# Kernel optimization log

Hardware: AMD Instinct MI355X
Metric: run time of the kernel (lower is better)

Reference implementation:

```python
import jax, jax.numpy as jnp
import numpy as np

NUM_OUT_POINTS = 2048  # matches init_kwargs num_out_points


def _fps_indices(x, m):
    """Farthest point sampling. x: [B, C, N] -> idx: [B, m] int32.
    Standard algorithm: seed at point 0, iteratively keep per-point min
    distance to the selected set and pick the argmax."""
    B, C, N = x.shape
    first = jnp.zeros((B,), dtype=jnp.int32)
    init_dists = jnp.full((B, N), jnp.inf, dtype=x.dtype)

    def body(carry, _):
        dists, last = carry                                   # [B,N], [B]
        last_pt = jnp.take_along_axis(x, last[:, None, None].astype(jnp.int32), axis=2)  # [B,C,1]
        d = jnp.sum((x - last_pt) ** 2, axis=1)               # [B,N] squared dist to newest point
        dists = jnp.minimum(dists, d)                         # min dist to selected set
        nxt = jnp.argmax(dists, axis=1).astype(jnp.int32)     # farthest point
        return (dists, nxt), nxt

    (_, _), rest = jax.lax.scan(body, (init_dists, first), None, length=m - 1)  # rest: [m-1, B]
    idx = jnp.concatenate([first[None, :], rest], axis=0)     # [m, B]
    return idx.T                                              # [B, m]


def setup_inputs() -> dict:
    key = jax.random.key(0)
    x = jax.random.normal(key, (32, 3, 131072), dtype=jnp.float32)
    return {"x": x}


def reference(x):
    # input_shape == output_shape == 'bcn', permute == False
    B, C, N = x.shape
    idx = _fps_indices(x, NUM_OUT_POINTS)                     # [B, M]
    gather_idx = jnp.broadcast_to(idx[:, None, :], (B, C, NUM_OUT_POINTS))
    y = jnp.take_along_axis(x, gather_idx, axis=2)            # [B, C, M]
    return y
```

## Files before the change

kernel.cpp:

```cpp
#include <hip/hip_runtime.h>
#include <stdint.h>


#define B_   32
#define N_   131072
#define M_   2048
#define WPB  8
#define T_   1024
#define PTS  16
#define ITERS (M_ - 1)
#define NPW  (N_ / WPB)

typedef unsigned long long u64;

__global__ void __launch_bounds__(T_, 4)
fps_main(const float* __restrict__ x, float* __restrict__ y,
         u64* __restrict__ slots) {
    const int bid  = blockIdx.x;
    const int b    = bid & (B_ - 1);
    const int wl   = bid >> 5;
    const int tid  = threadIdx.x;
    const int lane = tid & 63;
    const int wave = tid >> 6;

    const float* __restrict__ xb = x + (size_t)b * 3u * N_;
    float* __restrict__ yb = y + (size_t)b * 3u * M_;
    const unsigned pbase = (unsigned)(wl * NPW + tid);

    float X[PTS], Y[PTS], Z[PTS], D[PTS];
#pragma unroll
    for (int k = 0; k < PTS; ++k) {
        unsigned p = pbase + (unsigned)(k * T_);
        X[k] = xb[p];
        Y[k] = xb[N_ + p];
        Z[k] = xb[2 * N_ + p];
        D[k] = INFINITY;
    }

    float lx = xb[0], ly = xb[N_], lz = xb[2 * N_];
    if (wl == 0 && tid == 0) { yb[0] = lx; yb[M_] = ly; yb[2 * M_] = lz; }

    __shared__ u64   s_key[16];
    __shared__ float s_c[3];


    for (int it = 0; it < ITERS; ++it) {
        const int par = it & 1;

        float bv = -INFINITY; unsigned bi = 0u;
#pragma unroll
        for (int k = 0; k < PTS; ++k) {
            float dx = X[k] - lx;
            float dy = Y[k] - ly;
            float dz = Z[k] - lz;
            float d  = __fadd_rn(__fadd_rn(__fmul_rn(dx, dx), __fmul_rn(dy, dy)),
                                 __fmul_rn(dz, dz));
            float nd = fminf(D[k], d);
            D[k] = nd;
            bool t = nd > bv;
            bv = t ? nd : bv;
            bi = t ? (pbase + (unsigned)(k * T_)) : bi;
        }

        u64 key = ((u64)__float_as_uint(bv) << 32)
                | ((u64)(unsigned)it << 17)
                | (u64)(0x1FFFFu - bi);

#pragma unroll
        for (int off = 1; off < 64; off <<= 1) {
            u64 o = __shfl_xor(key, off);
            key = (o > key) ? o : key;
        }
        if (lane == 0) s_key[wave] = key;
        __syncthreads();

        if (wave == 0) {
            u64 k2 = (lane < 16) ? s_key[lane] : 0ull;
#pragma unroll
            for (int off = 1; off < 16; off <<= 1) {
                u64 o = __shfl_xor(k2, off);
                k2 = (o > k2) ? o : k2;
            }

            u64* base = slots + (size_t)((b * 2 + par) * WPB);
            if (lane == 0)
                __hip_atomic_store(base + wl, k2,
                                   __ATOMIC_RELAXED, __HIP_MEMORY_SCOPE_AGENT);

            const unsigned wtag = (unsigned)it;
            u64 got = 0ull;
            for (;;) {
                if (lane < WPB)
                    got = __hip_atomic_load(base + lane,
                                            __ATOMIC_RELAXED, __HIP_MEMORY_SCOPE_AGENT);
                bool ok = (lane >= WPB) | (((unsigned)(got >> 17) & 0x7FFFu) == wtag);
                if (__all(ok)) break;
                __builtin_amdgcn_s_sleep(2);
            }

            u64 w = (lane < WPB) ? got : 0ull;
#pragma unroll
            for (int off = 1; off < 8; off <<= 1) {
                u64 o = __shfl_xor(w, off);
                w = (o > w) ? o : w;
            }
            unsigned widx = 0x1FFFFu - (unsigned)(w & 0x1FFFFu);
            if (lane < 3) s_c[lane] = xb[(size_t)lane * N_ + widx];
        }
        __syncthreads();

        lx = s_c[0]; ly = s_c[1]; lz = s_c[2];
        if (wl == 0 && tid == 0) {
            yb[it + 1]          = lx;
            yb[M_ + it + 1]     = ly;
            yb[2 * M_ + it + 1] = lz;
        }
    }
}

extern "C" void kernel_launch(void* const* d_in, const int* in_sizes, int n_in,
                              void* d_out, int out_size, void* d_ws, size_t ws_size,
                              hipStream_t stream) {
    const float* x = (const float*)d_in[0];
    float* y = (float*)d_out;
    u64* slots = (u64*)d_ws;
    fps_main<<<B_ * WPB, T_, 0, stream>>>(x, y, slots);
}
```

Baseline: 5.579 ms.

## Replace block barriers with LDS flag sync and carry winner coordinates in records

The two __syncthreads per iteration are replaced by an LDS atomic counter that wave 0 spins on, plus a tag flag that the other waves spin on. Each block now publishes the winning point's coordinates together with its key in global slots, so the extra dependent global load of the winner's coordinates disappears. The s_sleep is also removed from the cross-block polling loop. Spin-waiting within a workgroup avoids barrier latency but burns issue slots and relies on the waves making forward progress. Polling 32 words instead of 8 adds memory traffic.

```diff
diff --git a/kernel.cpp b/kernel.cpp
--- a/kernel.cpp
+++ b/kernel.cpp
@@ -40,12 +40,17 @@
     float lx = xb[0], ly = xb[N_], lz = xb[2 * N_];
     if (wl == 0 && tid == 0) { yb[0] = lx; yb[M_] = ly; yb[2 * M_] = lz; }
 
-    __shared__ u64   s_key[16];
-    __shared__ float s_c[3];
+    __shared__ u64      s_rec[16][4];
+    __shared__ unsigned s_cnt;
+    __shared__ unsigned s_tag;
+    __shared__ float    s_c[3];
 
+    if (tid == 0) { s_cnt = 0u; s_tag = 0xFFFFFFFFu; }
+    __syncthreads();
 
     for (int it = 0; it < ITERS; ++it) {
         const int par = it & 1;
+        const unsigned ittag = (unsigned)it;
 
         float bv = -INFINITY; unsigned bi = 0u;
 #pragma unroll
@@ -63,57 +68,90 @@
         }
 
         u64 key = ((u64)__float_as_uint(bv) << 32)
-                | ((u64)(unsigned)it << 17)
+                | ((u64)ittag << 17)
                 | (u64)(0x1FFFFu - bi);
 
+        u64 wk = key;
 #pragma unroll
         for (int off = 1; off < 64; off <<= 1) {
-            u64 o = __shfl_xor(key, off);
-            key = (o > key) ? o : key;
+            u64 o = __shfl_xor(wk, off);
+            wk = (o > wk) ? o : wk;
         }
-        if (lane == 0) s_key[wave] = key;
-        __syncthreads();
+
+        if (key == wk) {
+            float bx = 0.f, by = 0.f, bz = 0.f;
+#pragma unroll
+            for (int k = 0; k < PTS; ++k)
+                if (pbase + (unsigned)(k * T_) == bi) { bx = X[k]; by = Y[k]; bz = Z[k]; }
+            s_rec[wave][0] = wk;
+            s_rec[wave][1] = ((u64)__float_as_uint(bx) << 32) | (u64)ittag;
+            s_rec[wave][2] = ((u64)__float_as_uint(by) << 32) | (u64)ittag;
+            s_rec[wave][3] = ((u64)__float_as_uint(bz) << 32) | (u64)ittag;
+            __hip_atomic_fetch_add(&s_cnt, 1u, __ATOMIC_RELEASE, __HIP_MEMORY_SCOPE_WORKGROUP);
+        }
 
         if (wave == 0) {
-            u64 k2 = (lane < 16) ? s_key[lane] : 0ull;
+            const unsigned want = 16u * (unsigned)(it + 1);
+            while (__hip_atomic_load(&s_cnt, __ATOMIC_ACQUIRE,
+                                     __HIP_MEMORY_SCOPE_WORKGROUP) < want) {}
+
+            u64 k2 = (lane < 16) ? s_rec[lane][0] : 0ull;
+            u64 m2 = k2;
 #pragma unroll
             for (int off = 1; off < 16; off <<= 1) {
-                u64 o = __shfl_xor(k2, off);
-                k2 = (o > k2) ? o : k2;
+                u64 o = __shfl_xor(m2, off);
+                m2 = (o > m2) ? o : m2;
+            }
+            u64 ball = __ballot(lane < 16 && k2 == m2);
+            int wv = __ffsll(ball) - 1;
+
+            u64* grec = slots + (size_t)(((b * 2 + par) * WPB + wl) * 4);
+            u64 word = 0ull;
+            if (lane == 0)      word = m2;
+            else if (lane < 4)  word = s_rec[wv][lane];
+            if (lane < 4)
+                __hip_atomic_store(&grec[lane], word,
+                                   __ATOMIC_RELAXED, __HIP_MEMORY_SCOPE_AGENT);
+
+            u64* gb = slots + (size_t)((b * 2 + par) * WPB * 4);
+            const int w = lane & 3;
+            u64 got = 0ull;
+            for (;;) {
+                if (lane < 32)
+                    got = __hip_atomic_load(&gb[lane],
+                                            __ATOMIC_RELAXED, __HIP_MEMORY_SCOPE_AGENT);
+                bool ok = (lane >= 32) |
+                          ((w == 0) ? (((unsigned)(got >> 17) & 0x7FFFu) == ittag)
+                                    : (((unsigned)got & 0x7FFFu) == ittag));
+                if (__all(ok)) break;
             }
 
-            u64* base = slots + (size_t)((b * 2 + par) * WPB);
-            if (lane == 0)
-                __hip_atomic_store(base + wl, k2,
-                                   __ATOMIC_RELAXED, __HIP_MEMORY_SCOPE_AGENT);
+            u64 kk = (lane < 32 && w == 0) ? got : 0ull;
+#pragma unroll
+            for (int off = 1; off < 64; off <<= 1) {
+                u64 o = __shfl_xor(kk, off);
+                kk = (o > kk) ? o : kk;
+            }
+            u64 ball2 = __ballot(lane < 32 && w == 0 && got == kk);
+            int winl = __ffsll(ball2) - 1;
+            lx = __uint_as_float((unsigned)(__shfl(got, winl + 1) >> 32));
+            ly = __uint_as_float((unsigned)(__shfl(got, winl + 2) >> 32));
+            lz = __uint_as_float((unsigned)(__shfl(got, winl + 3) >> 32));
 
-            const unsigned wtag = (unsigned)it;
-            u64 got = 0ull;
-            for (;;) {
-                if (lane < WPB)
-                    got = __hip_atomic_load(base + lane,
-                                            __ATOMIC_RELAXED, __HIP_MEMORY_SCOPE_AGENT);
-                bool ok = (lane >= WPB) | (((unsigned)(got >> 17) & 0x7FFFu) == wtag);
-                if (__all(ok)) break;
-                __builtin_amdgcn_s_sleep(2);
+            if (lane == 0) {
+                s_c[0] = lx; s_c[1] = ly; s_c[2] = lz;
+                __hip_atomic_store(&s_tag, ittag,
+                                   __ATOMIC_RELEASE, __HIP_MEMORY_SCOPE_WORKGROUP);
             }
-
-            u64 w = (lane < WPB) ? got : 0ull;
-#pragma unroll
-            for (int off = 1; off < 8; off <<= 1) {
-                u64 o = __shfl_xor(w, off);
-                w = (o > w) ? o : w;
+        } else {
+            while (__hip_atomic_load(&s_tag, __ATOMIC_ACQUIRE,
+                                     __HIP_MEMORY_SCOPE_WORKGROUP) != ittag) {}
+            lx = s_c[0]; ly = s_c[1]; lz = s_c[2];
+            if (wl == 0 && wave == 1 && lane == 0) {
+                yb[it + 1]          = lx;
+                yb[M_ + it + 1]     = ly;
+                yb[2 * M_ + it + 1] = lz;
             }
-            unsigned widx = 0x1FFFFu - (unsigned)(w & 0x1FFFFu);
-            if (lane < 3) s_c[lane] = xb[(size_t)lane * N_ + widx];
-        }
-        __syncthreads();
-
-        lx = s_c[0]; ly = s_c[1]; lz = s_c[2];
-        if (wl == 0 && tid == 0) {
-            yb[it + 1]          = lx;
-            yb[M_ + it + 1]     = ly;
-            yb[2 * M_ + it + 1] = lz;
         }
     }
 }
```

Measured after the change: 8.026 ms. +43.9%, slower.

## Interleave two batches per workgroup to hide cross-block sync latency

Applied to the files above, without the earlier changes.

Each workgroup now handles two batch elements (b and b+16), with 16 workgroups per batch pair instead of 8 per batch. The per-iteration global slot publish for batch A happens before computing batch B, so the cross-workgroup handshake latency of one batch can overlap the compute of the other. The grid size stays at 256 workgroups but the split per batch doubles, which widens the spin-wait fan-in to 16 slots. The spin sleep is also shortened.

```diff
diff --git a/kernel.cpp b/kernel.cpp
--- a/kernel.cpp
+++ b/kernel.cpp
@@ -2,118 +2,177 @@
 #include <stdint.h>
 
 
-#define B_   32
-#define N_   131072
-#define M_   2048
-#define WPB  8
-#define T_   1024
-#define PTS  16
+#define B_    32
+#define N_    131072
+#define M_    2048
+#define PAIRS 16
+#define WPB   16
+#define T_    1024
+#define PTS   8
 #define ITERS (M_ - 1)
-#define NPW  (N_ / WPB)
+#define NPW   (N_ / WPB)
 
 typedef unsigned long long u64;
+
+__device__ __forceinline__ u64 wave_max64(u64 v) {
+#pragma unroll
+    for (int off = 1; off < 64; off <<= 1) {
+        u64 o = __shfl_xor(v, off);
+        v = (o > v) ? o : v;
+    }
+    return v;
+}
 
 __global__ void __launch_bounds__(T_, 4)
 fps_main(const float* __restrict__ x, float* __restrict__ y,
          u64* __restrict__ slots) {
-    const int bid  = blockIdx.x;
-    const int b    = bid & (B_ - 1);
-    const int wl   = bid >> 5;
+    const int wg   = blockIdx.x;
+    const int pp   = wg & (PAIRS - 1);
+    const int wl   = wg >> 4;
+    const int bA   = pp;
+    const int bB   = pp + PAIRS;
     const int tid  = threadIdx.x;
     const int lane = tid & 63;
     const int wave = tid >> 6;
 
-    const float* __restrict__ xb = x + (size_t)b * 3u * N_;
-    float* __restrict__ yb = y + (size_t)b * 3u * M_;
+    const float* __restrict__ xA = x + (size_t)bA * 3u * N_;
+    const float* __restrict__ xB = x + (size_t)bB * 3u * N_;
+    float* __restrict__ yA = y + (size_t)bA * 3u * M_;
+    float* __restrict__ yB = y + (size_t)bB * 3u * M_;
     const unsigned pbase = (unsigned)(wl * NPW + tid);
 
-    float X[PTS], Y[PTS], Z[PTS], D[PTS];
+    float XA[PTS], YA[PTS], ZA[PTS], DA[PTS];
+    float XB[PTS], YB[PTS], ZB[PTS], DB[PTS];
 #pragma unroll
     for (int k = 0; k < PTS; ++k) {
         unsigned p = pbase + (unsigned)(k * T_);
-        X[k] = xb[p];
-        Y[k] = xb[N_ + p];
-        Z[k] = xb[2 * N_ + p];
-        D[k] = INFINITY;
+        XA[k] = xA[p]; YA[k] = xA[N_ + p]; ZA[k] = xA[2*N_ + p]; DA[k] = INFINITY;
+        XB[k] = xB[p]; YB[k] = xB[N_ + p]; ZB[k] = xB[2*N_ + p]; DB[k] = INFINITY;
     }
 
-    float lx = xb[0], ly = xb[N_], lz = xb[2 * N_];
-    if (wl == 0 && tid == 0) { yb[0] = lx; yb[M_] = ly; yb[2 * M_] = lz; }
+    float lxA = xA[0], lyA = xA[N_], lzA = xA[2*N_];
+    float lxB = xB[0], lyB = xB[N_], lzB = xB[2*N_];
+    if (wl == 0 && tid == 0) {
+        yA[0] = lxA; yA[M_] = lyA; yA[2*M_] = lzA;
+        yB[0] = lxB; yB[M_] = lyB; yB[2*M_] = lzB;
+    }
 
-    __shared__ u64   s_key[16];
-    __shared__ float s_c[3];
+    __shared__ u64   s_keyA[16], s_keyB[16];
+    __shared__ float s_cA[3], s_cB[3];
 
 
     for (int it = 0; it < ITERS; ++it) {
         const int par = it & 1;
+        const unsigned ittag = (unsigned)it;
 
-        float bv = -INFINITY; unsigned bi = 0u;
+        {
+            float bv = -INFINITY; unsigned bi = 0u;
 #pragma unroll
-        for (int k = 0; k < PTS; ++k) {
-            float dx = X[k] - lx;
-            float dy = Y[k] - ly;
-            float dz = Z[k] - lz;
-            float d  = __fadd_rn(__fadd_rn(__fmul_rn(dx, dx), __fmul_rn(dy, dy)),
-                                 __fmul_rn(dz, dz));
-            float nd = fminf(D[k], d);
-            D[k] = nd;
-            bool t = nd > bv;
-            bv = t ? nd : bv;
-            bi = t ? (pbase + (unsigned)(k * T_)) : bi;
+            for (int k = 0; k < PTS; ++k) {
+                float dx = XA[k]-lxA, dy = YA[k]-lyA, dz = ZA[k]-lzA;
+                float d  = __fadd_rn(__fadd_rn(__fmul_rn(dx,dx), __fmul_rn(dy,dy)),
+                                     __fmul_rn(dz,dz));
+                float nd = fminf(DA[k], d);
+                DA[k] = nd;
+                bool t = nd > bv;
+                bv = t ? nd : bv;
+                bi = t ? (pbase + (unsigned)(k * T_)) : bi;
+            }
+            u64 key = ((u64)__float_as_uint(bv) << 32)
+                    | ((u64)ittag << 17) | (u64)(0x1FFFFu - bi);
+            key = wave_max64(key);
+            if (lane == 0) s_keyA[wave] = key;
         }
-
-        u64 key = ((u64)__float_as_uint(bv) << 32)
-                | ((u64)(unsigned)it << 17)
-                | (u64)(0x1FFFFu - bi);
-
-#pragma unroll
-        for (int off = 1; off < 64; off <<= 1) {
-            u64 o = __shfl_xor(key, off);
-            key = (o > key) ? o : key;
-        }
-        if (lane == 0) s_key[wave] = key;
         __syncthreads();
 
         if (wave == 0) {
-            u64 k2 = (lane < 16) ? s_key[lane] : 0ull;
+            u64 k2 = (lane < 16) ? s_keyA[lane] : 0ull;
 #pragma unroll
             for (int off = 1; off < 16; off <<= 1) {
                 u64 o = __shfl_xor(k2, off);
                 k2 = (o > k2) ? o : k2;
             }
+            if (lane == 0)
+                __hip_atomic_store(slots + (size_t)((bA*2+par)*WPB + wl), k2,
+                                   __ATOMIC_RELAXED, __HIP_MEMORY_SCOPE_AGENT);
+        }
 
-            u64* base = slots + (size_t)((b * 2 + par) * WPB);
-            if (lane == 0)
-                __hip_atomic_store(base + wl, k2,
-                                   __ATOMIC_RELAXED, __HIP_MEMORY_SCOPE_AGENT);
-
-            const unsigned wtag = (unsigned)it;
-            u64 got = 0ull;
-            for (;;) {
-                if (lane < WPB)
-                    got = __hip_atomic_load(base + lane,
-                                            __ATOMIC_RELAXED, __HIP_MEMORY_SCOPE_AGENT);
-                bool ok = (lane >= WPB) | (((unsigned)(got >> 17) & 0x7FFFu) == wtag);
-                if (__all(ok)) break;
-                __builtin_amdgcn_s_sleep(2);
+        {
+            float bv = -INFINITY; unsigned bi = 0u;
+#pragma unroll
+            for (int k = 0; k < PTS; ++k) {
+                float dx = XB[k]-lxB, dy = YB[k]-lyB, dz = ZB[k]-lzB;
+                float d  = __fadd_rn(__fadd_rn(__fmul_rn(dx,dx), __fmul_rn(dy,dy)),
+                                     __fmul_rn(dz,dz));
+                float nd = fminf(DB[k], d);
+                DB[k] = nd;
+                bool t = nd > bv;
+                bv = t ? nd : bv;
+                bi = t ? (pbase + (unsigned)(k * T_)) : bi;
             }
-
-            u64 w = (lane < WPB) ? got : 0ull;
-#pragma unroll
-            for (int off = 1; off < 8; off <<= 1) {
-                u64 o = __shfl_xor(w, off);
-                w = (o > w) ? o : w;
-            }
-            unsigned widx = 0x1FFFFu - (unsigned)(w & 0x1FFFFu);
-            if (lane < 3) s_c[lane] = xb[(size_t)lane * N_ + widx];
+            u64 key = ((u64)__float_as_uint(bv) << 32)
+                    | ((u64)ittag << 17) | (u64)(0x1FFFFu - bi);
+            key = wave_max64(key);
+            if (lane == 0) s_keyB[wave] = key;
         }
         __syncthreads();
 
-        lx = s_c[0]; ly = s_c[1]; lz = s_c[2];
-        if (wl == 0 && tid == 0) {
-            yb[it + 1]          = lx;
-            yb[M_ + it + 1]     = ly;
-            yb[2 * M_ + it + 1] = lz;
+        if (wave == 0) {
+            u64 k2 = (lane < 16) ? s_keyB[lane] : 0ull;
+#pragma unroll
+            for (int off = 1; off < 16; off <<= 1) {
+                u64 o = __shfl_xor(k2, off);
+                k2 = (o > k2) ? o : k2;
+            }
+            if (lane == 0)
+                __hip_atomic_store(slots + (size_t)((bB*2+par)*WPB + wl), k2,
+                                   __ATOMIC_RELAXED, __HIP_MEMORY_SCOPE_AGENT);
+
+            u64* gbA = slots + (size_t)((bA*2+par)*WPB);
+            u64 gotA = 0ull;
+            for (;;) {
+                if (lane < WPB)
+                    gotA = __hip_atomic_load(gbA + lane,
+                                             __ATOMIC_RELAXED, __HIP_MEMORY_SCOPE_AGENT);
+                bool ok = (lane >= WPB) | (((unsigned)(gotA >> 17) & 0x7FFFu) == ittag);
+                if (__all(ok)) break;
+                __builtin_amdgcn_s_sleep(1);
+            }
+            u64 kA = (lane < WPB) ? gotA : 0ull;
+#pragma unroll
+            for (int off = 1; off < 16; off <<= 1) {
+                u64 o = __shfl_xor(kA, off);
+                kA = (o > kA) ? o : kA;
+            }
+            unsigned widxA = 0x1FFFFu - (unsigned)(kA & 0x1FFFFu);
+            if (lane < 3) s_cA[lane] = xA[(size_t)lane * N_ + widxA];
+
+            u64* gbB = slots + (size_t)((bB*2+par)*WPB);
+            u64 gotB = 0ull;
+            for (;;) {
+                if (lane < WPB)
+                    gotB = __hip_atomic_load(gbB + lane,
+                                             __ATOMIC_RELAXED, __HIP_MEMORY_SCOPE_AGENT);
+                bool ok = (lane >= WPB) | (((unsigned)(gotB >> 17) & 0x7FFFu) == ittag);
+                if (__all(ok)) break;
+                __builtin_amdgcn_s_sleep(1);
+            }
+            u64 kB = (lane < WPB) ? gotB : 0ull;
+#pragma unroll
+            for (int off = 1; off < 16; off <<= 1) {
+                u64 o = __shfl_xor(kB, off);
+                kB = (o > kB) ? o : kB;
+            }
+            unsigned widxB = 0x1FFFFu - (unsigned)(kB & 0x1FFFFu);
+            if (lane < 3) s_cB[lane] = xB[(size_t)lane * N_ + widxB];
+        }
+        __syncthreads();
+
+        lxA = s_cA[0]; lyA = s_cA[1]; lzA = s_cA[2];
+        lxB = s_cB[0]; lyB = s_cB[1]; lzB = s_cB[2];
+        if (wl == 0 && lane == 0) {
+            if (wave == 1) { yA[it+1] = lxA; yA[M_+it+1] = lyA; yA[2*M_+it+1] = lzA; }
+            if (wave == 2) { yB[it+1] = lxB; yB[M_+it+1] = lyB; yB[2*M_+it+1] = lzB; }
         }
     }
 }
@@ -124,5 +183,5 @@
     const float* x = (const float*)d_in[0];
     float* y = (float*)d_out;
     u64* slots = (u64*)d_ws;
-    fps_main<<<B_ * WPB, T_, 0, stream>>>(x, y, slots);
+    fps_main<<<B_ * WPB / 2, T_, 0, stream>>>(x, y, slots);
 }
```

New measurement: 7.471 ms. +33.9%, slower.
